# Optimization experiments

Hardware: AMD Instinct MI355X
Metric: run time of the kernel (lower is better)

## Reference

```python
import jax, jax.numpy as jnp
import numpy as np

# --- LIF neuron (spikingjelly LIFNode, single-step, tau=2.0, hard reset, ATan surrogate) ---
# With zero initial membrane potential, one step gives h = x / tau, spike = heaviside(h - v_th).
ALPHA = 2.0  # ATan surrogate default alpha
TAU = 2.0    # LIFNode default tau
V_TH = 1.0

@jax.custom_vjp
def atan_heaviside(x):
    return (x >= 0.0).astype(x.dtype)

def _ah_fwd(x):
    return (x >= 0.0).astype(x.dtype), x

def _ah_bwd(res, g):
    # d/dx of ATan surrogate: alpha / (2 * (1 + (pi/2 * alpha * x)^2))
    return (g * (ALPHA / (2.0 * (1.0 + (jnp.pi / 2.0 * ALPHA * res) ** 2))),)

atan_heaviside.defvjp(_ah_fwd, _ah_bwd)

def lif(x):
    return atan_heaviside(x / TAU - V_TH)

DIM, NUM_HEADS, TOPK = 256, 8, 4
WT, WH, WW = 2, 4, 4

def setup_inputs() -> dict:
    key = jax.random.key(0)
    k1, k2, k3, k4, k5 = jax.random.split(key, 5)
    T, B, Lt, Lh, Lw, C = 4, 2, 8, 32, 32, DIM
    x = jax.random.normal(k1, (T, B, Lt, Lh, Lw, C), dtype=jnp.float32)
    w_qkv = jax.random.normal(k2, (C, 3 * C), dtype=jnp.float32) * 0.02
    b_qkv = jax.random.normal(k3, (3 * C,), dtype=jnp.float32) * 0.02
    w_proj = jax.random.normal(k4, (C, C), dtype=jnp.float32) * 0.02
    b_proj = jax.random.normal(k5, (C,), dtype=jnp.float32) * 0.02
    return {"x": x, "w_qkv": w_qkv, "b_qkv": b_qkv, "w_proj": w_proj, "b_proj": b_proj}

def reference(x, w_qkv, b_qkv, w_proj, b_proj):
    T, B, Lt, Lh, Lw, C = x.shape
    H = NUM_HEADS
    D = C // H
    scale = D ** -0.5
    lt, lh, lw = Lt // WT, Lh // WH, Lw // WW
    W = WT * WH * WW          # num_wins = 32
    S = lt * lh * lw          # win_size = 256

    # window partition: [T,B,Lt,Lh,Lw,C] -> [T,B,W,S,C]
    xw = x.reshape(T, B, WT, lt, WH, lh, WW, lw, C)
    xw = xw.transpose(0, 1, 2, 4, 6, 3, 5, 7, 8).reshape(T, B, W, S, C)

    # region routing: mean over timesteps and tokens -> [B,W,C]
    region = xw.mean(axis=(0, 3))
    scores = jnp.einsum('bwc,bvc->bwv', region, region) * scale  # [B,W,W]
    idx = jax.lax.top_k(scores, TOPK)[1]                          # [B,W,K] int32

    # qkv projection + spiking activations
    qkv = xw @ w_qkv + b_qkv                                      # [T,B,W,S,3C]
    q, k, v = jnp.split(qkv, 3, axis=-1)
    q, k, v = lif(q), lif(k), lif(v)
    q = q.reshape(T, B, W, S, H, D)
    k = k.reshape(T, B, W, S, H, D)
    v = v.reshape(T, B, W, S, H, D)

    # gather routed KV blocks: k_g[t,b,w,j] = k[t,b,idx[b,w,j]]
    b_ix = jnp.arange(B)[:, None, None]
    k_g = k[:, b_ix, idx].reshape(T, B, W, TOPK * S, H, D)        # [T,B,W,K*S,H,D]
    v_g = v[:, b_ix, idx].reshape(T, B, W, TOPK * S, H, D)

    # linear attention: kv = k^T v, out = q @ kv, normalized by q @ sum(k)
    kv = jnp.einsum('tbwnhd,tbwnhe->tbwhde', k_g, v_g)            # [T,B,W,H,D,D]
    out = jnp.einsum('tbwshd,tbwhde->tbwshe', q, kv)              # [T,B,W,S,H,D]
    den = jnp.einsum('tbwshd,tbwhd->tbwsh', q, k_g.sum(axis=3))[..., None]
    out = out / (den + 1e-6)

    out = out.reshape(T, B, W, S, C) @ w_proj + b_proj

    # window reverse: [T,B,W,S,C] -> [T,B,Lt,Lh,Lw,C]
    out = out.reshape(T, B, WT, WH, WW, lt, lh, lw, C)
    out = out.transpose(0, 1, 2, 5, 3, 6, 4, 7, 8).reshape(T, B, Lt, Lh, Lw, C)
    return out
```

## Files before the change

### kernel.cpp

```cpp
#include <hip/hip_runtime.h>
#include <hip/hip_bf16.h>
#include <stdint.h>

#define NT 4
#define NB 2
#define NW 32
#define NS 256
#define NC 256
#define NH 8
#define ND 32
#define NK 4

typedef unsigned int u32;
typedef unsigned long long u64;
typedef unsigned short u16;
typedef __attribute__((ext_vector_type(8))) short bf16x8;
typedef __attribute__((ext_vector_type(4))) float f32x4;

__device__ __forceinline__ int wofs(int w) {
  return (w >> 4) * 4096 + ((w >> 2) & 3) * 256 + (w & 3) * 8;
}
__device__ __forceinline__ int sofs(int s) {
  return ((s >> 6) << 10) + (((s >> 3) & 7) << 5) + (s & 7);
}
__device__ __forceinline__ size_t x_off(int t, int b, int w, int s, int c) {
  return ((size_t)((t * NB + b) * 8192 + wofs(w) + sofs(s))) * NC + c;
}

__device__ __forceinline__ u32 f2bf(float f) {
  union { float f; u32 i; } u; u.f = f;
  return (u.i + 0x7FFFu + ((u.i >> 16) & 1u)) >> 16;
}

__device__ __forceinline__ void gload16(const u16* g, u16* l) {
  __builtin_amdgcn_global_load_lds(
      (const __attribute__((address_space(1))) void*)g,
      (__attribute__((address_space(3))) void*)l, 16, 0, 0);
}

__global__ __launch_bounds__(256) void k_prep(const float* __restrict__ x,
                                              const float* __restrict__ w_qkv,
                                              u16* __restrict__ xw,
                                              u16* __restrict__ bt,
                                              float* __restrict__ region) {
  int blk = blockIdx.x, tid = threadIdx.x;
  if (blk >= 512) {
    int n = (blk - 512) * 8 + (tid >> 5);
    int kc = tid & 31;
    u16 vals[8];
#pragma unroll
    for (int j = 0; j < 8; ++j)
      vals[j] = (u16)f2bf(w_qkv[(size_t)(kc * 8 + j) * 768 + n]);
    *reinterpret_cast<uint4*>(&bt[(size_t)n * 256 + kc * 8]) =
        *reinterpret_cast<const uint4*>(vals);
    return;
  }
  __shared__ float sums[4][4][NC];
  int g = tid >> 6, c4 = tid & 63;
  size_t base = (size_t)blk * 128;
  float4 s[4];
#pragma unroll
  for (int ww = 0; ww < 4; ++ww) s[ww] = make_float4(0.f, 0.f, 0.f, 0.f);
#pragma unroll
  for (int p = 0; p < 32; ++p) {
    int row = p * 4 + g;
    float4 v = *reinterpret_cast<const float4*>(&x[(base + row) * NC + c4 * 4]);
    uint2 bf;
    bf.x = f2bf(v.x) | (f2bf(v.y) << 16);
    bf.y = f2bf(v.z) | (f2bf(v.w) << 16);
    *reinterpret_cast<uint2*>(&xw[(base + row) * NC + c4 * 4]) = bf;
    int ww = (p & 7) >> 1;
    s[ww].x += v.x; s[ww].y += v.y; s[ww].z += v.z; s[ww].w += v.w;
  }
#pragma unroll
  for (int ww = 0; ww < 4; ++ww)
    *reinterpret_cast<float4*>(&sums[ww][g][c4 * 4]) = s[ww];
  __syncthreads();
  int b = (blk >> 6) & 1;
  int wt = ((blk >> 3) & 7) >> 2, wh = (blk & 7) >> 1;
  int v0 = wt * 16 + wh * 4;
  int c = tid;
#pragma unroll
  for (int ww = 0; ww < 4; ++ww) {
    float tot = (sums[ww][0][c] + sums[ww][1][c] + sums[ww][2][c] + sums[ww][3][c]) *
                (1.0f / 1024.0f);
    atomicAdd(&region[((size_t)b * NW + v0 + ww) * NC + c], tot);
  }
}

__global__ __launch_bounds__(256) void k_scores(const float* __restrict__ region,
                                                int* __restrict__ idx) {
  __shared__ float rs[NW][NC];
  __shared__ float scval[NW];
  int blk = blockIdx.x;
  int b = blk >> 5, w = blk & 31;
  int tid = threadIdx.x;
  for (int i = tid; i < NW * NC; i += 256)
    rs[i >> 8][i & 255] = region[(size_t)b * NW * NC + i];
  __syncthreads();
  int v = tid >> 3, l8 = tid & 7;
  float sum = 0.f;
  const float* a = rs[w];
  const float* bb = rs[v];
#pragma unroll
  for (int j = 0; j < 32; ++j) sum += a[l8 * 32 + j] * bb[l8 * 32 + j];
  sum += __shfl_xor(sum, 1);
  sum += __shfl_xor(sum, 2);
  sum += __shfl_xor(sum, 4);
  if (l8 == 0) scval[v] = sum * 0.17677669529663687f;
  __syncthreads();
  if (tid == 0) {
    float sc[NW];
#pragma unroll
    for (int j = 0; j < NW; ++j) sc[j] = scval[j];
    for (int kk = 0; kk < NK; ++kk) {
      float best = -__builtin_inff(); int bi = 0;
      for (int j = 0; j < NW; ++j)
        if (sc[j] > best) { best = sc[j]; bi = j; }
      idx[(b * NW + w) * NK + kk] = bi;
      sc[bi] = -__builtin_inff();
    }
  }
}

__global__ __launch_bounds__(256, 2) void k_gemm(const u16* __restrict__ xw,
                                                 const u16* __restrict__ bt,
                                                 const float* __restrict__ b_qkv,
                                                 u32* __restrict__ qb, u32* __restrict__ kb,
                                                 u32* __restrict__ vb,
                                                 u32* __restrict__ winflag) {
  __shared__ __align__(16) u16 As[2][128 * 32];
  __shared__ __align__(16) u16 Bs[2][256 * 32];
  __shared__ u32 wfl;

  const int tid = threadIdx.x;
  const int v = (blockIdx.x & 7) * 192 + (blockIdx.x >> 3);
  const int mt = v / 3, nt = v % 3;
  const int m0 = mt * 128, n0 = nt * 256;
  const int wave = tid >> 6, lane = tid & 63;
  const int wr = wave >> 1, wc = wave & 1;

  if (tid == 0) wfl = 0;

  const f32x4 vz = {0.f, 0.f, 0.f, 0.f};
  f32x4 acc[4][8];
#pragma unroll
  for (int m = 0; m < 4; ++m)
#pragma unroll
    for (int n = 0; n < 8; ++n) acc[m][n] = vz;

  auto stage = [&](int buf, int ks) {
    const int k0 = ks * 32;
#pragma unroll
    for (int p = 0; p < 2; ++p) {
      int cbase = (wave * 2 + p) * 64;
      int c = cbase + lane;
      int row = c >> 2, sl = c & 3;
      int ssl = sl ^ ((row >> 1) & 3);
      gload16(&xw[(size_t)(m0 + row) * 256 + k0 + ssl * 8], &As[buf][cbase * 8]);
    }
#pragma unroll
    for (int p = 0; p < 4; ++p) {
      int cbase = (wave * 4 + p) * 64;
      int c = cbase + lane;
      int row = c >> 2, sl = c & 3;
      int ssl = sl ^ ((row >> 1) & 3);
      gload16(&bt[(size_t)(n0 + row) * 256 + k0 + ssl * 8], &Bs[buf][cbase * 8]);
    }
  };

  stage(0, 0);
  __syncthreads();
#pragma unroll
  for (int ks = 0; ks < 8; ++ks) {
    const int buf = ks & 1;
    if (ks < 7) stage(buf ^ 1, ks + 1);
    bf16x8 afr[4], bfr[8];
#pragma unroll
    for (int m = 0; m < 4; ++m) {
      int r = wr * 64 + m * 16 + (lane & 15);
      int phys = (lane >> 4) ^ ((r >> 1) & 3);
      afr[m] = *reinterpret_cast<const bf16x8*>(&As[buf][r * 32 + phys * 8]);
    }
#pragma unroll
    for (int n = 0; n < 8; ++n) {
      int r = wc * 128 + n * 16 + (lane & 15);
      int phys = (lane >> 4) ^ ((r >> 1) & 3);
      bfr[n] = *reinterpret_cast<const bf16x8*>(&Bs[buf][r * 32 + phys * 8]);
    }
#pragma unroll
    for (int m = 0; m < 4; ++m)
#pragma unroll
      for (int n = 0; n < 8; ++n)
        acc[m][n] = __builtin_amdgcn_mfma_f32_16x16x32_bf16(afr[m], bfr[n], acc[m][n], 0, 0, 0);
    __syncthreads();
  }

  float bias[8];
#pragma unroll
  for (int n = 0; n < 8; ++n) bias[n] = b_qkv[n0 + wc * 128 + n * 16 + (lane & 15)];
  u32* dst = (nt == 0) ? qb : (nt == 1) ? kb : vb;
  const int g = lane >> 4;
  u32 wfl_loc = 0;
#pragma unroll
  for (int m = 0; m < 4; ++m)
#pragma unroll
    for (int r = 0; r < 4; ++r) {
      u32 words[4];
#pragma unroll
      for (int jp = 0; jp < 4; ++jp) {
        u64 b0 = __ballot(acc[m][2 * jp][r] + bias[2 * jp] >= 2.0f);
        u64 b1 = __ballot(acc[m][2 * jp + 1][r] + bias[2 * jp + 1] >= 2.0f);
        words[jp] = (u32)((b0 >> (g * 16)) & 0xFFFFu) |
                    ((u32)((b1 >> (g * 16)) & 0xFFFFu) << 16);
      }
      if ((lane & 15) < 4) {
        int jp = lane & 3;
        int row = wr * 64 + m * 16 + g * 4 + r;
        u32 wv = words[jp];
        dst[(size_t)(m0 + row) * NH + wc * 4 + jp] = wv;
        if (wv) wfl_loc |= 1u << ((row & 31) >> 3);
      }
    }
  if (wfl_loc) atomicOr(&wfl, wfl_loc);
  __syncthreads();
  if (tid == 0 && wfl) {
    int t = mt >> 7, b = (mt >> 6) & 1, Lt = (mt >> 3) & 7, hh = mt & 7;
    int w0 = (Lt >> 2) * 16 + (hh >> 1) * 4;
    u32 bit = 1u << nt;
    for (int ww = 0; ww < 4; ++ww)
      if (wfl & (1u << ww))
        atomicOr(&winflag[(t * NB + b) * NW + w0 + ww], bit);
  }
}

__global__ __launch_bounds__(256) void k_attn(const u32* __restrict__ qb,
                                              const u32* __restrict__ kb,
                                              const u32* __restrict__ vb,
                                              const int* __restrict__ idx,
                                              const u32* __restrict__ winflag,
                                              const float* __restrict__ w_proj,
                                              const float* __restrict__ b_proj,
                                              float* __restrict__ out) {
  __shared__ u32 qs[64 * NH];
  __shared__ unsigned short kvc[NH * ND * ND];
  __shared__ u32 ksum[NH * ND];
  __shared__ float attnrow[NC];

  int blk = blockIdx.x;
  int wid = blk >> 2, sc = blk & 3;
  int t = wid >> 6, b = (wid >> 5) & 1, w = wid & 31;
  int s0 = sc * 64;
  int tid = threadIdx.x;

  u32 fs = winflag[(t * NB + b) * NW + w];
  int wj[NK];
  u32 fk = 0, fv = 0;
#pragma unroll
  for (int j = 0; j < NK; ++j) {
    wj[j] = idx[(b * NW + w) * NK + j];
    u32 f = winflag[(t * NB + b) * NW + wj[j]];
    fk |= f & 2u; fv |= f & 4u;
  }
  bool skip = !(fs & 1u) || !fk || !fv;

  if (skip) {
    float bp = b_proj[tid];
    for (int s = s0; s < s0 + 64; ++s) out[x_off(t, b, w, s, tid)] = bp;
    return;
  }

  int tb = (t * NB + b) * 8192;
  size_t gb[NK];
#pragma unroll
  for (int j = 0; j < NK; ++j) gb[j] = (size_t)(tb + wofs(wj[j])) * NH;
  size_t qbase = (size_t)(tb + wofs(w)) * NH;
  for (int i = tid; i < 64 * NH; i += 256)
    qs[i] = qb[qbase + (size_t)sofs(s0 + (i >> 3)) * NH + (i & 7)];
  {
    int h = tid >> 5, d = tid & 31;
    u32 cnt = 0;
    for (int n = 0; n < NK * NS; ++n)
      cnt += (kb[gb[n >> 8] + (size_t)sofs(n & 255) * NH + h] >> d) & 1u;
    ksum[tid] = cnt;
  }
  for (int p = tid; p < NH * ND * ND; p += 256) {
    int h = p >> 10, d = (p >> 5) & 31, e = p & 31;
    u32 cnt = 0;
    for (int n = 0; n < NK * NS; ++n) {
      size_t a = gb[n >> 8] + (size_t)sofs(n & 255) * NH + h;
      cnt += ((kb[a] >> d) & (vb[a] >> e)) & 1u;
    }
    kvc[p] = (unsigned short)cnt;
  }
  __syncthreads();
  int h = tid >> 5, e = tid & 31;
  float bpv = b_proj[tid];
  for (int sl = 0; sl < 64; ++sl) {
    u32 qw = qs[sl * NH + h];
    float num = 0.f, den = 0.f;
    for (int d = 0; d < ND; ++d) {
      if ((qw >> d) & 1u) {
        den += (float)ksum[h * ND + d];
        num += (float)kvc[h * ND * ND + d * ND + e];
      }
    }
    attnrow[tid] = num / (den + 1e-6f);
    __syncthreads();
    float acc = bpv;
    for (int c = 0; c < NC; ++c) acc += attnrow[c] * w_proj[c * NC + tid];
    out[x_off(t, b, w, s0 + sl, tid)] = acc;
    __syncthreads();
  }
}

extern "C" void kernel_launch(void* const* d_in, const int* in_sizes, int n_in,
                              void* d_out, int out_size, void* d_ws, size_t ws_size,
                              hipStream_t stream) {
  const float* x      = (const float*)d_in[0];
  const float* w_qkv  = (const float*)d_in[1];
  const float* b_qkv  = (const float*)d_in[2];
  const float* w_proj = (const float*)d_in[3];
  const float* b_proj = (const float*)d_in[4];
  float* out = (float*)d_out;

  char* ws = (char*)d_ws;
  int* idx       = (int*)(ws + 0x200000);
  u16* bt        = (u16*)(ws + 0x201000);
  u32* winflag   = (u32*)(ws + 0x270000);
  float* region  = (float*)(ws + 0x271000);
  u32* qb        = (u32*)(ws + 0x300000);
  u32* kb        = qb + (size_t)NT * NB * NW * NS * NH;
  u32* vb        = kb + (size_t)NT * NB * NW * NS * NH;
  u16* xw        = (u16*)(ws + 0x900000);

  hipMemsetAsync(ws + 0x270000, 0, 0x11000, stream);
  k_prep<<<608, 256, 0, stream>>>(x, w_qkv, xw, bt, region);
  k_scores<<<NB * NW, 256, 0, stream>>>(region, idx);
  k_gemm<<<1536, 256, 0, stream>>>(xw, bt, b_qkv, qb, kb, vb, winflag);
  k_attn<<<NT * NB * NW * 4, 256, 0, stream>>>(qb, kb, vb, idx, winflag, w_proj, b_proj, out);
}
```

Before: 86.07 us.

## Fuse fp32-to-bf16 conversion and region means into QKV GEMM A-tile staging

Measured after the change: 87.70 us. Within noise of the previous version (+1.9%).

```diff
diff --git a/kernel.cpp b/kernel.cpp
--- a/kernel.cpp
+++ b/kernel.cpp
@@ -38,99 +38,28 @@
       (__attribute__((address_space(3))) void*)l, 16, 0, 0);
 }
 
-__global__ __launch_bounds__(256) void k_prep(const float* __restrict__ x,
-                                              const float* __restrict__ w_qkv,
-                                              u16* __restrict__ xw,
-                                              u16* __restrict__ bt,
-                                              float* __restrict__ region) {
-  int blk = blockIdx.x, tid = threadIdx.x;
-  if (blk >= 512) {
-    int n = (blk - 512) * 8 + (tid >> 5);
-    int kc = tid & 31;
-    u16 vals[8];
-#pragma unroll
-    for (int j = 0; j < 8; ++j)
-      vals[j] = (u16)f2bf(w_qkv[(size_t)(kc * 8 + j) * 768 + n]);
-    *reinterpret_cast<uint4*>(&bt[(size_t)n * 256 + kc * 8]) =
-        *reinterpret_cast<const uint4*>(vals);
-    return;
-  }
-  __shared__ float sums[4][4][NC];
-  int g = tid >> 6, c4 = tid & 63;
-  size_t base = (size_t)blk * 128;
-  float4 s[4];
-#pragma unroll
-  for (int ww = 0; ww < 4; ++ww) s[ww] = make_float4(0.f, 0.f, 0.f, 0.f);
-#pragma unroll
-  for (int p = 0; p < 32; ++p) {
-    int row = p * 4 + g;
-    float4 v = *reinterpret_cast<const float4*>(&x[(base + row) * NC + c4 * 4]);
-    uint2 bf;
-    bf.x = f2bf(v.x) | (f2bf(v.y) << 16);
-    bf.y = f2bf(v.z) | (f2bf(v.w) << 16);
-    *reinterpret_cast<uint2*>(&xw[(base + row) * NC + c4 * 4]) = bf;
-    int ww = (p & 7) >> 1;
-    s[ww].x += v.x; s[ww].y += v.y; s[ww].z += v.z; s[ww].w += v.w;
-  }
-#pragma unroll
-  for (int ww = 0; ww < 4; ++ww)
-    *reinterpret_cast<float4*>(&sums[ww][g][c4 * 4]) = s[ww];
-  __syncthreads();
-  int b = (blk >> 6) & 1;
-  int wt = ((blk >> 3) & 7) >> 2, wh = (blk & 7) >> 1;
-  int v0 = wt * 16 + wh * 4;
-  int c = tid;
-#pragma unroll
-  for (int ww = 0; ww < 4; ++ww) {
-    float tot = (sums[ww][0][c] + sums[ww][1][c] + sums[ww][2][c] + sums[ww][3][c]) *
-                (1.0f / 1024.0f);
-    atomicAdd(&region[((size_t)b * NW + v0 + ww) * NC + c], tot);
-  }
-}
-
-__global__ __launch_bounds__(256) void k_scores(const float* __restrict__ region,
-                                                int* __restrict__ idx) {
-  __shared__ float rs[NW][NC];
-  __shared__ float scval[NW];
-  int blk = blockIdx.x;
-  int b = blk >> 5, w = blk & 31;
-  int tid = threadIdx.x;
-  for (int i = tid; i < NW * NC; i += 256)
-    rs[i >> 8][i & 255] = region[(size_t)b * NW * NC + i];
-  __syncthreads();
-  int v = tid >> 3, l8 = tid & 7;
-  float sum = 0.f;
-  const float* a = rs[w];
-  const float* bb = rs[v];
-#pragma unroll
-  for (int j = 0; j < 32; ++j) sum += a[l8 * 32 + j] * bb[l8 * 32 + j];
-  sum += __shfl_xor(sum, 1);
-  sum += __shfl_xor(sum, 2);
-  sum += __shfl_xor(sum, 4);
-  if (l8 == 0) scval[v] = sum * 0.17677669529663687f;
-  __syncthreads();
-  if (tid == 0) {
-    float sc[NW];
-#pragma unroll
-    for (int j = 0; j < NW; ++j) sc[j] = scval[j];
-    for (int kk = 0; kk < NK; ++kk) {
-      float best = -__builtin_inff(); int bi = 0;
-      for (int j = 0; j < NW; ++j)
-        if (sc[j] > best) { best = sc[j]; bi = j; }
-      idx[(b * NW + w) * NK + kk] = bi;
-      sc[bi] = -__builtin_inff();
-    }
-  }
-}
-
-__global__ __launch_bounds__(256, 2) void k_gemm(const u16* __restrict__ xw,
+__global__ __launch_bounds__(256) void k_prepw(const float* __restrict__ w_qkv,
+                                               u16* __restrict__ bt) {
+  int n = blockIdx.x * 8 + (threadIdx.x >> 5);
+  int kc = threadIdx.x & 31;
+  u16 vals[8];
+#pragma unroll
+  for (int j = 0; j < 8; ++j)
+    vals[j] = (u16)f2bf(w_qkv[(size_t)(kc * 8 + j) * 768 + n]);
+  *reinterpret_cast<uint4*>(&bt[(size_t)n * 256 + kc * 8]) =
+      *reinterpret_cast<const uint4*>(vals);
+}
+
+__global__ __launch_bounds__(256, 2) void k_gemm(const float* __restrict__ x,
                                                  const u16* __restrict__ bt,
                                                  const float* __restrict__ b_qkv,
                                                  u32* __restrict__ qb, u32* __restrict__ kb,
                                                  u32* __restrict__ vb,
-                                                 u32* __restrict__ winflag) {
+                                                 u32* __restrict__ winflag,
+                                                 float* __restrict__ region) {
   __shared__ __align__(16) u16 As[2][128 * 32];
   __shared__ __align__(16) u16 Bs[2][256 * 32];
+  __shared__ float4 sums4[2][256];
   __shared__ u32 wfl;
 
   const int tid = threadIdx.x;
@@ -139,6 +68,9 @@
   const int m0 = mt * 128, n0 = nt * 256;
   const int wave = tid >> 6, lane = tid & 63;
   const int wr = wave >> 1, wc = wave & 1;
+  const bool doreg = (nt == 0);
+  const int rb = (mt >> 6) & 1;
+  const int v0 = (((mt >> 3) & 7) >> 2) * 16 + ((mt & 7) >> 1) * 4;
 
   if (tid == 0) wfl = 0;
 
@@ -151,20 +83,28 @@
 
   auto stage = [&](int buf, int ks) {
     const int k0 = ks * 32;
-#pragma unroll
-    for (int p = 0; p < 2; ++p) {
-      int cbase = (wave * 2 + p) * 64;
-      int c = cbase + lane;
-      int row = c >> 2, sl = c & 3;
-      int ssl = sl ^ ((row >> 1) & 3);
-      gload16(&xw[(size_t)(m0 + row) * 256 + k0 + ssl * 8], &As[buf][cbase * 8]);
-    }
+    const int c4 = tid & 7, rowid = tid >> 3;
+    const int sl = c4 >> 1, half = c4 & 1;
+    float4 sv = make_float4(0.f, 0.f, 0.f, 0.f);
+#pragma unroll
+    for (int p = 0; p < 4; ++p) {
+      int row = p * 32 + rowid;
+      float4 f = *reinterpret_cast<const float4*>(
+          &x[(size_t)(m0 + row) * NC + k0 + c4 * 4]);
+      if (doreg) { sv.x += f.x; sv.y += f.y; sv.z += f.z; sv.w += f.w; }
+      uint2 bf;
+      bf.x = f2bf(f.x) | (f2bf(f.y) << 16);
+      bf.y = f2bf(f.z) | (f2bf(f.w) << 16);
+      int phys = sl ^ ((row >> 1) & 3);
+      *reinterpret_cast<uint2*>(&As[buf][row * 32 + phys * 8 + half * 4]) = bf;
+    }
+    if (doreg) sums4[ks & 1][tid] = sv;
 #pragma unroll
     for (int p = 0; p < 4; ++p) {
       int cbase = (wave * 4 + p) * 64;
       int c = cbase + lane;
-      int row = c >> 2, sl = c & 3;
-      int ssl = sl ^ ((row >> 1) & 3);
+      int row = c >> 2, bsl = c & 3;
+      int ssl = bsl ^ ((row >> 1) & 3);
       gload16(&bt[(size_t)(n0 + row) * 256 + k0 + ssl * 8], &Bs[buf][cbase * 8]);
     }
   };
@@ -174,6 +114,18 @@
 #pragma unroll
   for (int ks = 0; ks < 8; ++ks) {
     const int buf = ks & 1;
+    if (doreg && (tid >> 5) == ks) {
+      int local = tid & 31, c4l = local >> 2, comp = local & 3;
+      const float* sp = reinterpret_cast<const float*>(&sums4[ks & 1][0]);
+#pragma unroll
+      for (int ww = 0; ww < 4; ++ww) {
+        float s = 0.f;
+#pragma unroll
+        for (int j = 0; j < 8; ++j) s += sp[((ww * 8 + j) * 8 + c4l) * 4 + comp];
+        atomicAdd(&region[(size_t)(rb * NW + v0 + ww) * NC + tid],
+                  s * (1.0f / 1024.0f));
+      }
+    }
     if (ks < 7) stage(buf ^ 1, ks + 1);
     bf16x8 afr[4], bfr[8];
 #pragma unroll
@@ -225,12 +177,46 @@
   if (wfl_loc) atomicOr(&wfl, wfl_loc);
   __syncthreads();
   if (tid == 0 && wfl) {
-    int t = mt >> 7, b = (mt >> 6) & 1, Lt = (mt >> 3) & 7, hh = mt & 7;
-    int w0 = (Lt >> 2) * 16 + (hh >> 1) * 4;
     u32 bit = 1u << nt;
+    int t = mt >> 7;
     for (int ww = 0; ww < 4; ++ww)
       if (wfl & (1u << ww))
-        atomicOr(&winflag[(t * NB + b) * NW + w0 + ww], bit);
+        atomicOr(&winflag[(t * NB + rb) * NW + v0 + ww], bit);
+  }
+}
+
+__global__ __launch_bounds__(256) void k_scores(const float* __restrict__ region,
+                                                int* __restrict__ idx) {
+  __shared__ float rs[NW][NC];
+  __shared__ float scval[NW];
+  int blk = blockIdx.x;
+  int b = blk >> 5, w = blk & 31;
+  int tid = threadIdx.x;
+  for (int i = tid; i < NW * NC; i += 256)
+    rs[i >> 8][i & 255] = region[(size_t)b * NW * NC + i];
+  __syncthreads();
+  int v = tid >> 3, l8 = tid & 7;
+  float sum = 0.f;
+  const float* a = rs[w];
+  const float* bb = rs[v];
+#pragma unroll
+  for (int j = 0; j < 32; ++j) sum += a[l8 * 32 + j] * bb[l8 * 32 + j];
+  sum += __shfl_xor(sum, 1);
+  sum += __shfl_xor(sum, 2);
+  sum += __shfl_xor(sum, 4);
+  if (l8 == 0) scval[v] = sum * 0.17677669529663687f;
+  __syncthreads();
+  if (tid == 0) {
+    float sc[NW];
+#pragma unroll
+    for (int j = 0; j < NW; ++j) sc[j] = scval[j];
+    for (int kk = 0; kk < NK; ++kk) {
+      float best = -__builtin_inff(); int bi = 0;
+      for (int j = 0; j < NW; ++j)
+        if (sc[j] > best) { best = sc[j]; bi = j; }
+      idx[(b * NW + w) * NK + kk] = bi;
+      sc[bi] = -__builtin_inff();
+    }
   }
 }
 
@@ -332,11 +318,10 @@
   u32* qb        = (u32*)(ws + 0x300000);
   u32* kb        = qb + (size_t)NT * NB * NW * NS * NH;
   u32* vb        = kb + (size_t)NT * NB * NW * NS * NH;
-  u16* xw        = (u16*)(ws + 0x900000);
-
-  hipMemsetAsync(ws + 0x270000, 0, 0x11000, stream);
-  k_prep<<<608, 256, 0, stream>>>(x, w_qkv, xw, bt, region);
+
+  (void)hipMemsetAsync(ws + 0x270000, 0, 0x11000, stream);
+  k_prepw<<<96, 256, 0, stream>>>(w_qkv, bt);
+  k_gemm<<<1536, 256, 0, stream>>>(x, bt, b_qkv, qb, kb, vb, winflag, region);
   k_scores<<<NB * NW, 256, 0, stream>>>(region, idx);
-  k_gemm<<<1536, 256, 0, stream>>>(xw, bt, b_qkv, qb, kb, vb, winflag);
   k_attn<<<NT * NB * NW * 4, 256, 0, stream>>>(qb, kb, vb, idx, winflag, w_proj, b_proj, out);
 }
```
